# Performance work log

Measured on AMD Instinct MI355X. Metric: run time of the kernel, lower is better.

Reference implementation:

```python
import jax, jax.numpy as jnp
import numpy as np

B, D, C, P = 1024, 768, 150, 64  # batch, in_feats, num_labels, proj2 dim
POS_M, NEG_M = 0.7, 1.4


def setup_inputs() -> dict:
    key = jax.random.key(0)
    ks = jax.random.split(key, 8)
    return {
        "x": jax.random.normal(ks[0], (B, D), jnp.float32),
        "lb": jax.random.randint(ks[1], (B,), 0, C + 1),
        "mem": jax.random.normal(ks[2], (C, D), jnp.float32),
        "fc_w": jax.random.normal(ks[3], (2 * D, 2 * D), jnp.float32) * 0.02,
        "fc_b": jnp.zeros((2 * D,), jnp.float32),
        "p1_w": jax.random.normal(ks[4], (1, 2 * D), jnp.float32) * 0.02,
        "p1_b": jnp.zeros((1,), jnp.float32),
        "p2_w": jax.random.normal(ks[5], (P, 2 * D), jnp.float32) * 0.02,
        "p2_b": jnp.zeros((P,), jnp.float32),
    }


def reference(x, lb, mem, fc_w, fc_b, p1_w, p1_b, p2_w, p2_b):
    d = x.shape[1]
    # cat([a, b], 1) @ fc_w.T == a @ Wx.T + b @ Wm.T  (exact split of the linear)
    Wx, Wm = fc_w[:, :d], fc_w[:, d:]
    xh = x @ Wx.T + fc_b                                # [B, 2D]

    # --- get_logit ---
    seen_h = jax.nn.relu(xh[:, None, :] + mem @ Wm.T)   # [B, C, 2D]
    seen = jnp.einsum('bce,e->bc', seen_h, p1_w[0]) + p1_b[0]   # [B, C]
    uh = jax.nn.relu(xh)                                # cat([x, zeros]) path
    unseen = uh @ p1_w.T + p1_b                         # [B, 1]
    logits = jnp.concatenate([seen, unseen], axis=1)    # [B, C+1]

    # --- masked log-softmax losses (pos_adapte) ---
    labels = jax.nn.one_hot(lb, C + 1, dtype=jnp.float32)
    th = jnp.zeros_like(labels).at[:, -1].set(1.0)
    labels = labels.at[:, -1].set(0.0)
    p_mask = labels + th
    n_mask = 1.0 - labels
    BIG = 1e30
    loss1 = -(jax.nn.log_softmax(logits - (1.0 - p_mask) * BIG, -1) * labels).sum(1)
    loss2 = -(jax.nn.log_softmax(logits - (1.0 - n_mask) * BIG, -1) * th).sum(1)
    loss_cls = (loss1 + loss2).mean()

    # --- metric loss on unseen embedding ---
    u = uh @ p2_w.T + p2_b                              # [B, 64]
    u = u / jnp.maximum(jnp.linalg.norm(u, axis=1, keepdims=True), 1e-12)
    sq_n = (u * u).sum(1)
    sq = sq_n[:, None] + sq_n[None, :] - 2.0 * (u @ u.T)
    err = sq <= 0.0
    dist = jnp.sqrt(jnp.clip(sq, 1e-16, None)) * (~err).astype(u.dtype)
    same = lb[:, None] == lb[None, :]
    eye = jnp.eye(dist.shape[0], dtype=bool)
    pos = (same & ~eye).astype(dist.dtype)
    neg = (~same).astype(dist.dtype)
    pos_l = (jax.nn.relu(dist - POS_M) * pos).sum() / jnp.maximum(pos.sum(), 1.0)
    neg_l = (jax.nn.relu(NEG_M - dist) * neg).sum() / jnp.maximum(neg.sum(), 1.0)

    return loss_cls + pos_l + neg_l
```

## Files before the change

### kernel.cpp

```cpp
#include <hip/hip_runtime.h>
#include <math.h>

#define B_    1024
#define D_    768
#define C_    150
#define P_    64
#define TWOD  1536
#define NCLS  151
#define CPAD  256

#define ECHUNKS 16
#define ECHUNK  96

#define ASTR  40
#define USTRU 120
#define USTR  72

#define OFF_MH      0
#define OFF_XH      (OFF_MH + (C_ * TWOD) / 2)
#define OFF_PARTIAL (OFF_XH + (B_ * TWOD) / 2)
#define OFF_UHF     (OFF_PARTIAL + ECHUNKS * B_ * CPAD)
#define OFF_SQN     (OFF_UHF + (B_ * P_) / 2)
#define OFF_CLS     (OFF_SQN + B_)
#define OFF_PAIR    (OFF_CLS + B_)
#define OFF_XBF     (OFF_PAIR + 1024)
#define OFF_MEMBF   (OFF_XBF + (B_ * D_) / 2)
#define OFF_WBF     (OFF_MEMBF + (C_ * D_) / 2)
#define OFF_P2H     (OFF_WBF + (TWOD * TWOD) / 2)
#define OFF_P1H     (OFF_P2H + (P_ * TWOD) / 2)

typedef __bf16    bfx8   __attribute__((ext_vector_type(8)));
typedef _Float16  fp16x8 __attribute__((ext_vector_type(8)));
typedef _Float16  h2v    __attribute__((ext_vector_type(2)));
typedef float     f32x4  __attribute__((ext_vector_type(4)));

__device__ inline ushort f2bf(float f) {
    union { float f; unsigned u; } c; c.f = f;
    unsigned r = c.u + 0x7fffu + ((c.u >> 16) & 1u);
    return (ushort)(r >> 16);
}
__device__ inline ushort f2h(float f) {
    _Float16 h = (_Float16)f;
    return __builtin_bit_cast(ushort, h);
}
__device__ inline unsigned addrelu2(unsigned a, unsigned m) {
    h2v s = __builtin_bit_cast(h2v, a) + __builtin_bit_cast(h2v, m);
    h2v z = {(_Float16)0.f, (_Float16)0.f};
    s = __builtin_elementwise_max(s, z);
    return __builtin_bit_cast(unsigned, s);
}
__device__ inline unsigned relu2(unsigned a) {
    h2v s = __builtin_bit_cast(h2v, a);
    h2v z = {(_Float16)0.f, (_Float16)0.f};
    s = __builtin_elementwise_max(s, z);
    return __builtin_bit_cast(unsigned, s);
}
__device__ inline float dot2acc(unsigned a, unsigned b, float c) {
    return __builtin_amdgcn_fdot2(__builtin_bit_cast(h2v, a),
                                  __builtin_bit_cast(h2v, b), c, false);
}

#define X4   (B_ * D_ / 4)
#define MEM4 (C_ * D_ / 4)
#define W4   (TWOD * TWOD / 4)
#define P24  (P_ * TWOD / 4)
#define P14  (TWOD / 4)
#define TOT4 (X4 + MEM4 + W4 + P24 + P14)

__global__ __launch_bounds__(256) void prep_cvt(
    const float* __restrict__ x, const float* __restrict__ mem,
    const float* __restrict__ w, const float* __restrict__ p2w,
    const float* __restrict__ p1w,
    ushort* __restrict__ xb, ushort* __restrict__ memb,
    ushort* __restrict__ wb, ushort* __restrict__ p2h,
    ushort* __restrict__ p1h)
{
    int i = blockIdx.x * 256 + threadIdx.x;
    if (i >= TOT4) return;
    const float* src; ushort* dst; int off; bool bf;
    if (i < X4)                        { src = x;   dst = xb;   off = i; bf = true; }
    else if (i < X4 + MEM4)            { src = mem; dst = memb; off = i - X4; bf = true; }
    else if (i < X4 + MEM4 + W4)       { src = w;   dst = wb;   off = i - X4 - MEM4; bf = true; }
    else if (i < X4 + MEM4 + W4 + P24) { src = p2w; dst = p2h;  off = i - X4 - MEM4 - W4; bf = false; }
    else                               { src = p1w; dst = p1h;  off = i - X4 - MEM4 - W4 - P24; bf = false; }
    float4 v = ((const float4*)src)[off];
    ushort4 o;
    if (bf) { o.x = f2bf(v.x); o.y = f2bf(v.y); o.z = f2bf(v.z); o.w = f2bf(v.w); }
    else    { o.x = f2h(v.x);  o.y = f2h(v.y);  o.z = f2h(v.z);  o.w = f2h(v.w); }
    ((ushort4*)dst)[off] = o;
}

__global__ __launch_bounds__(256) void gemm_all(
    const ushort* __restrict__ xbf, const ushort* __restrict__ membf,
    const ushort* __restrict__ wbf, const float* __restrict__ fc_b,
    ushort* __restrict__ xh, ushort* __restrict__ mh)
{
    __shared__ ushort As[64 * ASTR];
    __shared__ ushort Bs[128 * ASTR];
    const int id = blockIdx.x;
    const int t  = threadIdx.x;

    const ushort* A; ushort* Out; int M, m0, n0, koff; bool xblk;
    if (id < 192) {
        xblk = true;  A = xbf;  Out = xh; M = B_;
        m0 = (id & 15) * 64; n0 = (id >> 4) * 128; koff = 0;
    } else {
        int q = id - 192;
        xblk = false; A = membf; Out = mh; M = C_;
        m0 = (q % 3) * 64; n0 = (q / 3) * 128; koff = D_;
    }

    const int wave = t >> 6, lane = t & 63;
    const int wm = (wave & 1) * 32, wn = (wave >> 1) * 64;
    const int fm = lane & 15, quad = lane >> 4;

    const int row_a = t >> 2, qa = (t & 3) * 8;
    const int ar = min(m0 + row_a, M - 1);
    const ushort* Arow = A + (size_t)ar * D_ + qa;
    const ushort* Brow = wbf + (size_t)(n0 + row_a) * TWOD + koff + qa;

    f32x4 acc[2][4];
#pragma unroll
    for (int j = 0; j < 4; ++j) {
        float bv = xblk ? fc_b[n0 + wn + j * 16 + fm] : 0.f;
#pragma unroll
        for (int i = 0; i < 2; ++i)
            acc[i][j] = (f32x4){bv, bv, bv, bv};
    }

    uint4 pa  = *(const uint4*)(Arow);
    uint4 pb0 = *(const uint4*)(Brow);
    uint4 pb1 = *(const uint4*)(Brow + 64 * TWOD);

    for (int k0 = 0; k0 < D_; k0 += 32) {
        __syncthreads();
        *(uint4*)&As[row_a * ASTR + qa] = pa;
        *(uint4*)&Bs[row_a * ASTR + qa] = pb0;
        *(uint4*)&Bs[(64 + row_a) * ASTR + qa] = pb1;
        __syncthreads();
        if (k0 + 32 < D_) {
            pa  = *(const uint4*)(Arow + k0 + 32);
            pb0 = *(const uint4*)(Brow + k0 + 32);
            pb1 = *(const uint4*)(Brow + 64 * TWOD + k0 + 32);
        }
        bfx8 af[2], bf[4];
#pragma unroll
        for (int i = 0; i < 2; ++i)
            af[i] = *(const bfx8*)&As[(wm + i * 16 + fm) * ASTR + quad * 8];
#pragma unroll
        for (int j = 0; j < 4; ++j)
            bf[j] = *(const bfx8*)&Bs[(wn + j * 16 + fm) * ASTR + quad * 8];
#pragma unroll
        for (int i = 0; i < 2; ++i)
#pragma unroll
            for (int j = 0; j < 4; ++j)
                acc[i][j] = __builtin_amdgcn_mfma_f32_16x16x32_bf16(
                    af[i], bf[j], acc[i][j], 0, 0, 0);
    }

#pragma unroll
    for (int i = 0; i < 2; ++i)
#pragma unroll
        for (int j = 0; j < 4; ++j)
#pragma unroll
            for (int r = 0; r < 4; ++r) {
                int row = m0 + wm + i * 16 + quad * 4 + r;
                int col = n0 + wn + j * 16 + fm;
                if (row < M) Out[(size_t)row * TWOD + col] = f2h(acc[i][j][r]);
            }
}

__global__ __launch_bounds__(256) void fused_tile(
    const ushort* __restrict__ xh, const ushort* __restrict__ mh,
    const ushort* __restrict__ p1h, const ushort* __restrict__ p2h,
    float* __restrict__ partial)
{
    __shared__ __align__(16) char smem[46080];
    const int t  = threadIdx.x;
    const int b0 = blockIdx.x * 128;
    const int z  = blockIdx.z;
    const int e0 = z * ECHUNK;

    if (blockIdx.y == 3) {
        ushort* Au = (ushort*)smem;
        ushort* Wu = (ushort*)(smem + 30720);
        const int wave = t >> 6, lane = t & 63;
        const int fm = lane & 15, quad = lane >> 4;

        {
            const int row = t >> 1, kh = (t & 1) * 48;
            const ushort* src = xh + (size_t)(b0 + row) * TWOD + e0 + kh;
            uint4 v[6];
#pragma unroll
            for (int i = 0; i < 6; ++i) v[i] = *(const uint4*)&src[i * 8];
#pragma unroll
            for (int i = 0; i < 6; ++i) {
                v[i].x = relu2(v[i].x); v[i].y = relu2(v[i].y);
                v[i].z = relu2(v[i].z); v[i].w = relu2(v[i].w);
                *(uint4*)&Au[row * USTRU + kh + i * 8] = v[i];
            }
        }
        {
            const int row = t >> 2, ks = (t & 3) * 24;
            const ushort* pw = p2h + (size_t)row * TWOD + e0 + ks;
#pragma unroll
            for (int i = 0; i < 3; ++i)
                *(uint4*)&Wu[row * USTRU + ks + i * 8] = *(const uint4*)&pw[i * 8];
        }
        __syncthreads();

        f32x4 uacc[2][4];
#pragma unroll
        for (int i = 0; i < 2; ++i)
#pragma unroll
            for (int j = 0; j < 4; ++j) uacc[i][j] = (f32x4){0.f, 0.f, 0.f, 0.f};
#pragma unroll
        for (int k0 = 0; k0 < ECHUNK; k0 += 32) {
            fp16x8 af[2], bf[4];
#pragma unroll
            for (int i = 0; i < 2; ++i)
                af[i] = *(const fp16x8*)&Au[(wave * 32 + i * 16 + fm) * USTRU + k0 + quad * 8];
#pragma unroll
            for (int j = 0; j < 4; ++j)
                bf[j] = *(const fp16x8*)&Wu[(j * 16 + fm) * USTRU + k0 + quad * 8];
#pragma unroll
            for (int i = 0; i < 2; ++i)
#pragma unroll
                for (int j = 0; j < 4; ++j)
                    uacc[i][j] = __builtin_amdgcn_mfma_f32_16x16x32_f16(
                        af[i], bf[j], uacc[i][j], 0, 0, 0);
        }
#pragma unroll
        for (int i = 0; i < 2; ++i)
#pragma unroll
            for (int j = 0; j < 4; ++j)
#pragma unroll
                for (int r = 0; r < 4; ++r) {
                    int row = b0 + wave * 32 + i * 16 + quad * 4 + r;
                    partial[((size_t)z * B_ + row) * CPAD + 192 + j * 16 + fm] =
                        uacc[i][j][r];
                }
        return;
    }

    unsigned* xT = (unsigned*)smem;
    unsigned* mT = (unsigned*)(smem + 24576);
    unsigned* wT = (unsigned*)(smem + 36864);
    const int c0 = blockIdx.y * 64;
    const int tm = t & 15, tn = t >> 4;

    {
        const int row = t >> 1, ph = (t & 1) * 48;
        const ushort* src = xh + (size_t)(b0 + row) * TWOD + e0 + ph;
        uint4 v[6];
#pragma unroll
        for (int i = 0; i < 6; ++i) v[i] = *(const uint4*)&src[i * 8];
#pragma unroll
        for (int i = 0; i < 6; ++i) {
            const int ep = (t & 1) * 24 + i * 4;
            xT[(ep + 0) * 128 + row] = v[i].x;
            xT[(ep + 1) * 128 + row] = v[i].y;
            xT[(ep + 2) * 128 + row] = v[i].z;
            xT[(ep + 3) * 128 + row] = v[i].w;
        }
    }
    {
        const int col = t & 63, seg = t >> 6;
        const int gc  = c0 + col;
        uint4 v[3];
        if (gc < C_) {
            const ushort* src = mh + (size_t)gc * TWOD + e0 + seg * 24;
#pragma unroll
            for (int i = 0; i < 3; ++i) v[i] = *(const uint4*)&src[i * 8];
        } else {
#pragma unroll
            for (int i = 0; i < 3; ++i) v[i] = make_uint4(0, 0, 0, 0);
        }
#pragma unroll
        for (int i = 0; i < 3; ++i) {
            const int ep = seg * 12 + i * 4;
            mT[(ep + 0) * 64 + col] = v[i].x;
            mT[(ep + 1) * 64 + col] = v[i].y;
            mT[(ep + 2) * 64 + col] = v[i].z;
            mT[(ep + 3) * 64 + col] = v[i].w;
        }
    }
    if (t < 12) {
        uint4 v = *(const uint4*)&p1h[e0 + t * 8];
        wT[t * 4 + 0] = v.x; wT[t * 4 + 1] = v.y;
        wT[t * 4 + 2] = v.z; wT[t * 4 + 3] = v.w;
    }
    __syncthreads();

    float acc[8][4] = {};
#pragma unroll 4
    for (int ep = 0; ep < 48; ++ep) {
        uint4 a0 = *(const uint4*)&xT[ep * 128 + tm * 8];
        uint4 a1 = *(const uint4*)&xT[ep * 128 + tm * 8 + 4];
        uint4 mj = *(const uint4*)&mT[ep * 64 + tn * 4];
        const unsigned wv = wT[ep];
        const unsigned aa[8] = {a0.x, a0.y, a0.z, a0.w, a1.x, a1.y, a1.z, a1.w};
        const unsigned mm[4] = {mj.x, mj.y, mj.z, mj.w};
#pragma unroll
        for (int i = 0; i < 8; ++i)
#pragma unroll
            for (int j = 0; j < 4; ++j)
                acc[i][j] = dot2acc(addrelu2(aa[i], mm[j]), wv, acc[i][j]);
    }

#pragma unroll
    for (int i = 0; i < 8; ++i) {
        const int gb = b0 + tm * 8 + i;
        float4 v = make_float4(acc[i][0], acc[i][1], acc[i][2], acc[i][3]);
        *(float4*)&partial[((size_t)z * B_ + gb) * CPAD + c0 + tn * 4] = v;
    }
}

__global__ __launch_bounds__(256) void reduce_row(
    const float* __restrict__ partial,
    const float* __restrict__ p1b, const float* __restrict__ p2b,
    const int* __restrict__ lb,
    ushort* __restrict__ uhf, float* __restrict__ sqn,
    float* __restrict__ clsbuf)
{
    const int b = blockIdx.x, t = threadIdx.x;
    float v = 0.f;
#pragma unroll
    for (int z = 0; z < ECHUNKS; ++z)
        v += partial[((size_t)z * B_ + b) * CPAD + t];
    if (t < NCLS)       v += p1b[0];
    else if (t >= 192)  v += p2b[t - 192];

    __shared__ float sval[256];
    sval[t] = v;
    __syncthreads();

    if (t < 64) {
        float uv = sval[192 + t];
        float s = uv * uv;
#pragma unroll
        for (int off = 32; off; off >>= 1) s += __shfl_xor(s, off);
        float inv = 1.f / fmaxf(sqrtf(s), 1e-12f);
        uhf[(size_t)b * P_ + t] = f2h(uv * inv);
        if (t == 0) sqn[b] = s * inv * inv;

        const int l = lb[b];
        float mx = -1e30f;
        for (int j = t; j < NCLS; j += 64)
            if (!(j == l && l < C_)) mx = fmaxf(mx, sval[j]);
#pragma unroll
        for (int off = 32; off; off >>= 1) mx = fmaxf(mx, __shfl_xor(mx, off));
        float se = 0.f;
        for (int j = t; j < NCLS; j += 64)
            if (!(j == l && l < C_)) se += expf(sval[j] - mx);
#pragma unroll
        for (int off = 32; off; off >>= 1) se += __shfl_xor(se, off);

        if (t == 0) {
            float l150  = sval[C_];
            float loss2 = mx + logf(se) - l150;
            float loss1 = 0.f;
            if (l < C_) {
                float a  = sval[l];
                float m2 = fmaxf(a, l150);
                loss1 = m2 - a + logf(expf(a - m2) + expf(l150 - m2));
            }
            clsbuf[b] = loss1 + loss2;
        }
    }
}

__global__ __launch_bounds__(256) void pair_loss(
    const ushort* __restrict__ uhf, const float* __restrict__ sqn,
    const int* __restrict__ lb, float* __restrict__ pairpart)
{
    __shared__ ushort ui_s[64 * USTR];
    __shared__ ushort uj_s[64 * USTR];
    __shared__ float sni[64], snj[64];
    __shared__ int   li[64],  lj[64];
    __shared__ float red[4][4];

    const int t  = threadIdx.x;
    const int i0 = blockIdx.x * 64, j0 = blockIdx.y * 64;

    for (int idx = t; idx < 512; idx += 256) {
        int row = idx >> 3, ch = (idx & 7) * 8;
        *(uint4*)&ui_s[row * USTR + ch] =
            *(const uint4*)&uhf[(size_t)(i0 + row) * P_ + ch];
        *(uint4*)&uj_s[row * USTR + ch] =
            *(const uint4*)&uhf[(size_t)(j0 + row) * P_ + ch];
    }
    if (t < 64)       { sni[t] = sqn[i0 + t]; li[t] = lb[i0 + t]; }
    else if (t < 128) { int q = t - 64; snj[q] = sqn[j0 + q]; lj[q] = lb[j0 + q]; }
    __syncthreads();

    const int wave = t >> 6, lane = t & 63;
    const int n = lane & 15, quad = lane >> 4;
    const int iw = wave * 16;

    const fp16x8 af0 = *(const fp16x8*)&ui_s[(iw + n) * USTR + quad * 8];
    const fp16x8 af1 = *(const fp16x8*)&ui_s[(iw + n) * USTR + quad * 8 + 32];

    f32x4 acc[4];
#pragma unroll
    for (int jt = 0; jt < 4; ++jt) {
        const fp16x8 bf0 = *(const fp16x8*)&uj_s[(jt * 16 + n) * USTR + quad * 8];
        const fp16x8 bf1 = *(const fp16x8*)&uj_s[(jt * 16 + n) * USTR + quad * 8 + 32];
        acc[jt] = __builtin_amdgcn_mfma_f32_16x16x32_f16(
            af0, bf0, (f32x4){0.f, 0.f, 0.f, 0.f}, 0, 0, 0);
        acc[jt] = __builtin_amdgcn_mfma_f32_16x16x32_f16(
            af1, bf1, acc[jt], 0, 0, 0);
    }

    float ps = 0.f, pc = 0.f, ns = 0.f, nc = 0.f;
#pragma unroll
    for (int jt = 0; jt < 4; ++jt)
#pragma unroll
        for (int r = 0; r < 4; ++r) {
            const int il = iw + quad * 4 + r;
            const int jl = jt * 16 + n;
            float sq = sni[il] + snj[jl] - 2.f * acc[jt][r];
            float dist = sq > 0.f ? sqrtf(fmaxf(sq, 1e-16f)) : 0.f;
            bool same = (li[il] == lj[jl]);
            if (same) {
                if (i0 + il != j0 + jl) { ps += fmaxf(dist - 0.7f, 0.f); pc += 1.f; }
            } else {
                ns += fmaxf(1.4f - dist, 0.f); nc += 1.f;
            }
        }

#pragma unroll
    for (int off = 32; off; off >>= 1) {
        ps += __shfl_xor(ps, off); pc += __shfl_xor(pc, off);
        ns += __shfl_xor(ns, off); nc += __shfl_xor(nc, off);
    }
    if (lane == 0) { red[0][wave] = ps; red[1][wave] = pc;
                     red[2][wave] = ns; red[3][wave] = nc; }
    __syncthreads();
    if (t == 0) {
        float4 v;
        v.x = red[0][0] + red[0][1] + red[0][2] + red[0][3];
        v.y = red[1][0] + red[1][1] + red[1][2] + red[1][3];
        v.z = red[2][0] + red[2][1] + red[2][2] + red[2][3];
        v.w = red[3][0] + red[3][1] + red[3][2] + red[3][3];
        *(float4*)&pairpart[(size_t)(blockIdx.y * 16 + blockIdx.x) * 4] = v;
    }
}

__global__ __launch_bounds__(256) void finalize(
    const float* __restrict__ clsbuf, const float* __restrict__ pairpart,
    float* __restrict__ out)
{
    __shared__ float red[5][4];
    const int t = threadIdx.x;
    float c = clsbuf[t] + clsbuf[t + 256] + clsbuf[t + 512] + clsbuf[t + 768];
    float4 pp = *(const float4*)&pairpart[(size_t)t * 4];
    float ps = pp.x, pc = pp.y, ns = pp.z, nc = pp.w;
#pragma unroll
    for (int off = 32; off; off >>= 1) {
        c  += __shfl_xor(c, off);
        ps += __shfl_xor(ps, off); pc += __shfl_xor(pc, off);
        ns += __shfl_xor(ns, off); nc += __shfl_xor(nc, off);
    }
    const int wave = t >> 6, lane = t & 63;
    if (lane == 0) { red[0][wave] = c; red[1][wave] = ps; red[2][wave] = pc;
                     red[3][wave] = ns; red[4][wave] = nc; }
    __syncthreads();
    if (t == 0) {
        float C = 0.f, PS = 0.f, PC = 0.f, NS = 0.f, NC = 0.f;
#pragma unroll
        for (int w = 0; w < 4; ++w) {
            C += red[0][w]; PS += red[1][w]; PC += red[2][w];
            NS += red[3][w]; NC += red[4][w];
        }
        out[0] = C / (float)B_ + PS / fmaxf(PC, 1.f) + NS / fmaxf(NC, 1.f);
    }
}

extern "C" void kernel_launch(void* const* d_in, const int* in_sizes, int n_in,
                              void* d_out, int out_size, void* d_ws, size_t ws_size,
                              hipStream_t stream)
{
    const float* x    = (const float*)d_in[0];
    const int*   lb   = (const int*)d_in[1];
    const float* mem  = (const float*)d_in[2];
    const float* fc_w = (const float*)d_in[3];
    const float* fc_b = (const float*)d_in[4];
    const float* p1w  = (const float*)d_in[5];
    const float* p1b  = (const float*)d_in[6];
    const float* p2w  = (const float*)d_in[7];
    const float* p2b  = (const float*)d_in[8];

    float* ws       = (float*)d_ws;
    ushort* mh      = (ushort*)(ws + OFF_MH);
    ushort* xh      = (ushort*)(ws + OFF_XH);
    float* partials = ws + OFF_PARTIAL;
    ushort* uhf     = (ushort*)(ws + OFF_UHF);
    float* sqn      = ws + OFF_SQN;
    float* clsbuf   = ws + OFF_CLS;
    float* pairpart = ws + OFF_PAIR;
    ushort* xbf     = (ushort*)(ws + OFF_XBF);
    ushort* membf   = (ushort*)(ws + OFF_MEMBF);
    ushort* wbf     = (ushort*)(ws + OFF_WBF);
    ushort* p2h     = (ushort*)(ws + OFF_P2H);
    ushort* p1h     = (ushort*)(ws + OFF_P1H);

    prep_cvt<<<(TOT4 + 255) / 256, 256, 0, stream>>>(x, mem, fc_w, p2w, p1w,
                                                     xbf, membf, wbf, p2h, p1h);
    gemm_all<<<228, 256, 0, stream>>>(xbf, membf, wbf, fc_b, xh, mh);
    fused_tile<<<dim3(8, 4, ECHUNKS), 256, 0, stream>>>(xh, mh, p1h, p2h,
                                                        partials);
    reduce_row<<<B_, 256, 0, stream>>>(partials, p1b, p2b, lb, uhf, sqn, clsbuf);
    pair_loss<<<dim3(16, 16), 256, 0, stream>>>(uhf, sqn, lb, pairpart);
    finalize<<<1, 256, 0, stream>>>(clsbuf, pairpart, (float*)d_out);
}
```

Measured before the change: 129.8 us.

## Fuse all six kernels into one persistent kernel with grid barriers

```diff
diff --git a/kernel.cpp b/kernel.cpp
--- a/kernel.cpp
+++ b/kernel.cpp
@@ -15,6 +15,8 @@
 #define ASTR  40
 #define USTRU 120
 #define USTR  72
+
+#define NBLK  512
 
 #define OFF_MH      0
 #define OFF_XH      (OFF_MH + (C_ * TWOD) / 2)
@@ -28,6 +30,7 @@
 #define OFF_WBF     (OFF_MEMBF + (C_ * D_) / 2)
 #define OFF_P2H     (OFF_WBF + (TWOD * TWOD) / 2)
 #define OFF_P1H     (OFF_P2H + (P_ * TWOD) / 2)
+#define OFF_BAR     (OFF_P1H + TWOD / 2)
 
 typedef __bf16    bfx8   __attribute__((ext_vector_type(8)));
 typedef _Float16  fp16x8 __attribute__((ext_vector_type(8)));
@@ -58,6 +61,35 @@
 __device__ inline float dot2acc(unsigned a, unsigned b, float c) {
     return __builtin_amdgcn_fdot2(__builtin_bit_cast(h2v, a),
                                   __builtin_bit_cast(h2v, b), c, false);
+}
+
+__device__ __forceinline__ void grid_barrier(int* bar)
+{
+    __syncthreads();
+    if (threadIdx.x == 0) {
+        int* gen = bar + 1;
+        const int g = __hip_atomic_load(gen, __ATOMIC_RELAXED,
+                                        __HIP_MEMORY_SCOPE_AGENT);
+        int* gcnt = bar + 16 + (blockIdx.x >> 4) * 16;
+        int gv = __hip_atomic_fetch_add(gcnt, 1, __ATOMIC_ACQ_REL,
+                                        __HIP_MEMORY_SCOPE_AGENT);
+        if (gv == 15) {
+            __hip_atomic_store(gcnt, 0, __ATOMIC_RELAXED,
+                               __HIP_MEMORY_SCOPE_AGENT);
+            int rv = __hip_atomic_fetch_add(bar, 1, __ATOMIC_ACQ_REL,
+                                            __HIP_MEMORY_SCOPE_AGENT);
+            if (rv == 31) {
+                __hip_atomic_store(bar, 0, __ATOMIC_RELAXED,
+                                   __HIP_MEMORY_SCOPE_AGENT);
+                __hip_atomic_fetch_add(gen, 1, __ATOMIC_RELEASE,
+                                       __HIP_MEMORY_SCOPE_AGENT);
+            }
+        }
+        while (__hip_atomic_load(gen, __ATOMIC_ACQUIRE,
+                                 __HIP_MEMORY_SCOPE_AGENT) == g)
+            __builtin_amdgcn_s_sleep(1);
+    }
+    __syncthreads();
 }
 
 #define X4   (B_ * D_ / 4)
@@ -67,7 +99,7 @@
 #define P14  (TWOD / 4)
 #define TOT4 (X4 + MEM4 + W4 + P24 + P14)
 
-__global__ __launch_bounds__(256) void prep_cvt(
+__device__ __forceinline__ void phase_cvt(
     const float* __restrict__ x, const float* __restrict__ mem,
     const float* __restrict__ w, const float* __restrict__ p2w,
     const float* __restrict__ p1w,
@@ -75,30 +107,31 @@
     ushort* __restrict__ wb, ushort* __restrict__ p2h,
     ushort* __restrict__ p1h)
 {
-    int i = blockIdx.x * 256 + threadIdx.x;
-    if (i >= TOT4) return;
-    const float* src; ushort* dst; int off; bool bf;
-    if (i < X4)                        { src = x;   dst = xb;   off = i; bf = true; }
-    else if (i < X4 + MEM4)            { src = mem; dst = memb; off = i - X4; bf = true; }
-    else if (i < X4 + MEM4 + W4)       { src = w;   dst = wb;   off = i - X4 - MEM4; bf = true; }
-    else if (i < X4 + MEM4 + W4 + P24) { src = p2w; dst = p2h;  off = i - X4 - MEM4 - W4; bf = false; }
-    else                               { src = p1w; dst = p1h;  off = i - X4 - MEM4 - W4 - P24; bf = false; }
-    float4 v = ((const float4*)src)[off];
-    ushort4 o;
-    if (bf) { o.x = f2bf(v.x); o.y = f2bf(v.y); o.z = f2bf(v.z); o.w = f2bf(v.w); }
-    else    { o.x = f2h(v.x);  o.y = f2h(v.y);  o.z = f2h(v.z);  o.w = f2h(v.w); }
-    ((ushort4*)dst)[off] = o;
-}
-
-__global__ __launch_bounds__(256) void gemm_all(
+    for (int i = blockIdx.x * 256 + threadIdx.x; i < TOT4; i += NBLK * 256) {
+        const float* src; ushort* dst; int off; bool bf;
+        if (i < X4)                        { src = x;   dst = xb;   off = i; bf = true; }
+        else if (i < X4 + MEM4)            { src = mem; dst = memb; off = i - X4; bf = true; }
+        else if (i < X4 + MEM4 + W4)       { src = w;   dst = wb;   off = i - X4 - MEM4; bf = true; }
+        else if (i < X4 + MEM4 + W4 + P24) { src = p2w; dst = p2h;  off = i - X4 - MEM4 - W4; bf = false; }
+        else                               { src = p1w; dst = p1h;  off = i - X4 - MEM4 - W4 - P24; bf = false; }
+        float4 v = ((const float4*)src)[off];
+        ushort4 o;
+        if (bf) { o.x = f2bf(v.x); o.y = f2bf(v.y); o.z = f2bf(v.z); o.w = f2bf(v.w); }
+        else    { o.x = f2h(v.x);  o.y = f2h(v.y);  o.z = f2h(v.z);  o.w = f2h(v.w); }
+        ((ushort4*)dst)[off] = o;
+    }
+}
+
+__device__ __forceinline__ void phase_gemm(
+    int id, char* smemc,
     const ushort* __restrict__ xbf, const ushort* __restrict__ membf,
     const ushort* __restrict__ wbf, const float* __restrict__ fc_b,
     ushort* __restrict__ xh, ushort* __restrict__ mh)
 {
-    __shared__ ushort As[64 * ASTR];
-    __shared__ ushort Bs[128 * ASTR];
-    const int id = blockIdx.x;
-    const int t  = threadIdx.x;
+    if (id >= 228) return;
+    ushort* As = (ushort*)smemc;
+    ushort* Bs = (ushort*)(smemc + 64 * ASTR * 2);
+    const int t = threadIdx.x;
 
     const ushort* A; ushort* Out; int M, m0, n0, koff; bool xblk;
     if (id < 192) {
@@ -143,19 +176,19 @@
             pb0 = *(const uint4*)(Brow + k0 + 32);
             pb1 = *(const uint4*)(Brow + 64 * TWOD + k0 + 32);
         }
-        bfx8 af[2], bf[4];
+        bfx8 af[2], bff[4];
 #pragma unroll
         for (int i = 0; i < 2; ++i)
             af[i] = *(const bfx8*)&As[(wm + i * 16 + fm) * ASTR + quad * 8];
 #pragma unroll
         for (int j = 0; j < 4; ++j)
-            bf[j] = *(const bfx8*)&Bs[(wn + j * 16 + fm) * ASTR + quad * 8];
+            bff[j] = *(const bfx8*)&Bs[(wn + j * 16 + fm) * ASTR + quad * 8];
 #pragma unroll
         for (int i = 0; i < 2; ++i)
 #pragma unroll
             for (int j = 0; j < 4; ++j)
                 acc[i][j] = __builtin_amdgcn_mfma_f32_16x16x32_bf16(
-                    af[i], bf[j], acc[i][j], 0, 0, 0);
+                    af[i], bff[j], acc[i][j], 0, 0, 0);
     }
 
 #pragma unroll
@@ -170,18 +203,19 @@
             }
 }
 
-__global__ __launch_bounds__(256) void fused_tile(
+__device__ __forceinline__ void phase_fused(
+    int id, char* smem,
     const ushort* __restrict__ xh, const ushort* __restrict__ mh,
     const ushort* __restrict__ p1h, const ushort* __restrict__ p2h,
     float* __restrict__ partial)
 {
-    __shared__ __align__(16) char smem[46080];
     const int t  = threadIdx.x;
-    const int b0 = blockIdx.x * 128;
-    const int z  = blockIdx.z;
+    const int b0 = (id & 7) * 128;
+    const int y  = (id >> 3) & 3;
+    const int z  = id >> 5;
     const int e0 = z * ECHUNK;
 
-    if (blockIdx.y == 3) {
+    if (y == 3) {
         ushort* Au = (ushort*)smem;
         ushort* Wu = (ushort*)(smem + 30720);
         const int wave = t >> 6, lane = t & 63;
@@ -216,19 +250,19 @@
             for (int j = 0; j < 4; ++j) uacc[i][j] = (f32x4){0.f, 0.f, 0.f, 0.f};
 #pragma unroll
         for (int k0 = 0; k0 < ECHUNK; k0 += 32) {
-            fp16x8 af[2], bf[4];
+            fp16x8 af[2], bff[4];
 #pragma unroll
             for (int i = 0; i < 2; ++i)
                 af[i] = *(const fp16x8*)&Au[(wave * 32 + i * 16 + fm) * USTRU + k0 + quad * 8];
 #pragma unroll
             for (int j = 0; j < 4; ++j)
-                bf[j] = *(const fp16x8*)&Wu[(j * 16 + fm) * USTRU + k0 + quad * 8];
+                bff[j] = *(const fp16x8*)&Wu[(j * 16 + fm) * USTRU + k0 + quad * 8];
 #pragma unroll
             for (int i = 0; i < 2; ++i)
 #pragma unroll
                 for (int j = 0; j < 4; ++j)
                     uacc[i][j] = __builtin_amdgcn_mfma_f32_16x16x32_f16(
-                        af[i], bf[j], uacc[i][j], 0, 0, 0);
+                        af[i], bff[j], uacc[i][j], 0, 0, 0);
         }
 #pragma unroll
         for (int i = 0; i < 2; ++i)
@@ -246,7 +280,7 @@
     unsigned* xT = (unsigned*)smem;
     unsigned* mT = (unsigned*)(smem + 24576);
     unsigned* wT = (unsigned*)(smem + 36864);
-    const int c0 = blockIdx.y * 64;
+    const int c0 = y * 64;
     const int tm = t & 15, tn = t >> 4;
 
     {
@@ -316,72 +350,80 @@
     }
 }
 
-__global__ __launch_bounds__(256) void reduce_row(
+__device__ __forceinline__ void phase_reduce(
+    char* smemc,
     const float* __restrict__ partial,
     const float* __restrict__ p1b, const float* __restrict__ p2b,
     const int* __restrict__ lb,
     ushort* __restrict__ uhf, float* __restrict__ sqn,
     float* __restrict__ clsbuf)
 {
-    const int b = blockIdx.x, t = threadIdx.x;
-    float v = 0.f;
-#pragma unroll
-    for (int z = 0; z < ECHUNKS; ++z)
-        v += partial[((size_t)z * B_ + b) * CPAD + t];
-    if (t < NCLS)       v += p1b[0];
-    else if (t >= 192)  v += p2b[t - 192];
-
-    __shared__ float sval[256];
-    sval[t] = v;
-    __syncthreads();
-
-    if (t < 64) {
-        float uv = sval[192 + t];
-        float s = uv * uv;
-#pragma unroll
-        for (int off = 32; off; off >>= 1) s += __shfl_xor(s, off);
-        float inv = 1.f / fmaxf(sqrtf(s), 1e-12f);
-        uhf[(size_t)b * P_ + t] = f2h(uv * inv);
-        if (t == 0) sqn[b] = s * inv * inv;
-
-        const int l = lb[b];
-        float mx = -1e30f;
-        for (int j = t; j < NCLS; j += 64)
-            if (!(j == l && l < C_)) mx = fmaxf(mx, sval[j]);
-#pragma unroll
-        for (int off = 32; off; off >>= 1) mx = fmaxf(mx, __shfl_xor(mx, off));
-        float se = 0.f;
-        for (int j = t; j < NCLS; j += 64)
-            if (!(j == l && l < C_)) se += expf(sval[j] - mx);
-#pragma unroll
-        for (int off = 32; off; off >>= 1) se += __shfl_xor(se, off);
-
-        if (t == 0) {
-            float l150  = sval[C_];
-            float loss2 = mx + logf(se) - l150;
-            float loss1 = 0.f;
-            if (l < C_) {
-                float a  = sval[l];
-                float m2 = fmaxf(a, l150);
-                loss1 = m2 - a + logf(expf(a - m2) + expf(l150 - m2));
+    float* sval = (float*)smemc;
+    const int t = threadIdx.x;
+    for (int b = blockIdx.x; b < B_; b += NBLK) {
+        float v = 0.f;
+#pragma unroll
+        for (int z = 0; z < ECHUNKS; ++z)
+            v += partial[((size_t)z * B_ + b) * CPAD + t];
+        if (t < NCLS)       v += p1b[0];
+        else if (t >= 192)  v += p2b[t - 192];
+
+        sval[t] = v;
+        __syncthreads();
+
+        if (t < 64) {
+            float uv = sval[192 + t];
+            float s = uv * uv;
+#pragma unroll
+            for (int off = 32; off; off >>= 1) s += __shfl_xor(s, off);
+            float inv = 1.f / fmaxf(sqrtf(s), 1e-12f);
+            uhf[(size_t)b * P_ + t] = f2h(uv * inv);
+            if (t == 0) sqn[b] = s * inv * inv;
+
+            const int l = lb[b];
+            float mx = -1e30f;
+            for (int j = t; j < NCLS; j += 64)
+                if (!(j == l && l < C_)) mx = fmaxf(mx, sval[j]);
+#pragma unroll
+            for (int off = 32; off; off >>= 1) mx = fmaxf(mx, __shfl_xor(mx, off));
+            float se = 0.f;
+            for (int j = t; j < NCLS; j += 64)
+                if (!(j == l && l < C_)) se += expf(sval[j] - mx);
+#pragma unroll
+            for (int off = 32; off; off >>= 1) se += __shfl_xor(se, off);
+
+            if (t == 0) {
+                float l150  = sval[C_];
+                float loss2 = mx + logf(se) - l150;
+                float loss1 = 0.f;
+                if (l < C_) {
+                    float a  = sval[l];
+                    float m2 = fmaxf(a, l150);
+                    loss1 = m2 - a + logf(expf(a - m2) + expf(l150 - m2));
+                }
+                clsbuf[b] = loss1 + loss2;
             }
-            clsbuf[b] = loss1 + loss2;
-        }
-    }
-}
-
-__global__ __launch_bounds__(256) void pair_loss(
+        }
+        __syncthreads();
+    }
+}
+
+__device__ __forceinline__ void phase_pair(
+    int id, char* smemc,
     const ushort* __restrict__ uhf, const float* __restrict__ sqn,
     const int* __restrict__ lb, float* __restrict__ pairpart)
 {
-    __shared__ ushort ui_s[64 * USTR];
-    __shared__ ushort uj_s[64 * USTR];
-    __shared__ float sni[64], snj[64];
-    __shared__ int   li[64],  lj[64];
-    __shared__ float red[4][4];
+    if (id >= 256) return;
+    ushort* ui_s = (ushort*)smemc;
+    ushort* uj_s = (ushort*)(smemc + 9216);
+    float*  sni  = (float*)(smemc + 18432);
+    float*  snj  = (float*)(smemc + 18688);
+    int*    li   = (int*)(smemc + 18944);
+    int*    lj   = (int*)(smemc + 19200);
+    float*  red  = (float*)(smemc + 19456);
 
     const int t  = threadIdx.x;
-    const int i0 = blockIdx.x * 64, j0 = blockIdx.y * 64;
+    const int i0 = (id & 15) * 64, j0 = (id >> 4) * 64;
 
     for (int idx = t; idx < 512; idx += 256) {
         int row = idx >> 3, ch = (idx & 7) * 8;
@@ -434,24 +476,26 @@
         ps += __shfl_xor(ps, off); pc += __shfl_xor(pc, off);
         ns += __shfl_xor(ns, off); nc += __shfl_xor(nc, off);
     }
-    if (lane == 0) { red[0][wave] = ps; red[1][wave] = pc;
-                     red[2][wave] = ns; red[3][wave] = nc; }
+    if (lane == 0) { red[0 * 4 + wave] = ps; red[1 * 4 + wave] = pc;
+                     red[2 * 4 + wave] = ns; red[3 * 4 + wave] = nc; }
     __syncthreads();
     if (t == 0) {
         float4 v;
-        v.x = red[0][0] + red[0][1] + red[0][2] + red[0][3];
-        v.y = red[1][0] + red[1][1] + red[1][2] + red[1][3];
-        v.z = red[2][0] + red[2][1] + red[2][2] + red[2][3];
-        v.w = red[3][0] + red[3][1] + red[3][2] + red[3][3];
-        *(float4*)&pairpart[(size_t)(blockIdx.y * 16 + blockIdx.x) * 4] = v;
-    }
-}
-
-__global__ __launch_bounds__(256) void finalize(
+        v.x = red[0] + red[1] + red[2] + red[3];
+        v.y = red[4] + red[5] + red[6] + red[7];
+        v.z = red[8] + red[9] + red[10] + red[11];
+        v.w = red[12] + red[13] + red[14] + red[15];
+        *(float4*)&pairpart[(size_t)id * 4] = v;
+    }
+}
+
+__device__ __forceinline__ void phase_final(
+    char* smemc,
     const float* __restrict__ clsbuf, const float* __restrict__ pairpart,
     float* __restrict__ out)
 {
-    __shared__ float red[5][4];
+    if (blockIdx.x != 0) return;
+    float* red = (float*)smemc;
     const int t = threadIdx.x;
     float c = clsbuf[t] + clsbuf[t + 256] + clsbuf[t + 512] + clsbuf[t + 768];
     float4 pp = *(const float4*)&pairpart[(size_t)t * 4];
@@ -463,18 +507,58 @@
         ns += __shfl_xor(ns, off); nc += __shfl_xor(nc, off);
     }
     const int wave = t >> 6, lane = t & 63;
-    if (lane == 0) { red[0][wave] = c; red[1][wave] = ps; red[2][wave] = pc;
-                     red[3][wave] = ns; red[4][wave] = nc; }
+    if (lane == 0) { red[0 * 4 + wave] = c; red[1 * 4 + wave] = ps;
+                     red[2 * 4 + wave] = pc; red[3 * 4 + wave] = ns;
+                     red[4 * 4 + wave] = nc; }
     __syncthreads();
     if (t == 0) {
         float C = 0.f, PS = 0.f, PC = 0.f, NS = 0.f, NC = 0.f;
 #pragma unroll
         for (int w = 0; w < 4; ++w) {
-            C += red[0][w]; PS += red[1][w]; PC += red[2][w];
-            NS += red[3][w]; NC += red[4][w];
+            C += red[0 * 4 + w]; PS += red[1 * 4 + w]; PC += red[2 * 4 + w];
+            NS += red[3 * 4 + w]; NC += red[4 * 4 + w];
         }
         out[0] = C / (float)B_ + PS / fmaxf(PC, 1.f) + NS / fmaxf(NC, 1.f);
     }
+}
+
+__global__ __launch_bounds__(256, 2) void mega(
+    const float* __restrict__ x, const int* __restrict__ lb,
+    const float* __restrict__ mem, const float* __restrict__ fc_w,
+    const float* __restrict__ fc_b, const float* __restrict__ p1w,
+    const float* __restrict__ p1b, const float* __restrict__ p2w,
+    const float* __restrict__ p2b,
+    float* ws, float* out)
+{
+    __shared__ __align__(16) char smem[46080];
+
+    ushort* mh       = (ushort*)(ws + OFF_MH);
+    ushort* xh       = (ushort*)(ws + OFF_XH);
+    float*  partial  = ws + OFF_PARTIAL;
+    ushort* uhf      = (ushort*)(ws + OFF_UHF);
+    float*  sqn      = ws + OFF_SQN;
+    float*  clsbuf   = ws + OFF_CLS;
+    float*  pairpart = ws + OFF_PAIR;
+    ushort* xbf      = (ushort*)(ws + OFF_XBF);
+    ushort* membf    = (ushort*)(ws + OFF_MEMBF);
+    ushort* wbf      = (ushort*)(ws + OFF_WBF);
+    ushort* p2h      = (ushort*)(ws + OFF_P2H);
+    ushort* p1h      = (ushort*)(ws + OFF_P1H);
+    int*    bar      = (int*)(ws + OFF_BAR);
+
+    const int id = blockIdx.x;
+
+    phase_cvt(x, mem, fc_w, p2w, p1w, xbf, membf, wbf, p2h, p1h);
+    grid_barrier(bar);
+    phase_gemm(id, smem, xbf, membf, wbf, fc_b, xh, mh);
+    grid_barrier(bar);
+    phase_fused(id, smem, xh, mh, p1h, p2h, partial);
+    grid_barrier(bar);
+    phase_reduce(smem, partial, p1b, p2b, lb, uhf, sqn, clsbuf);
+    grid_barrier(bar);
+    phase_pair(id, smem, uhf, sqn, lb, pairpart);
+    grid_barrier(bar);
+    phase_final(smem, clsbuf, pairpart, out);
 }
 
 extern "C" void kernel_launch(void* const* d_in, const int* in_sizes, int n_in,
@@ -491,26 +575,11 @@
     const float* p2w  = (const float*)d_in[7];
     const float* p2b  = (const float*)d_in[8];
 
-    float* ws       = (float*)d_ws;
-    ushort* mh      = (ushort*)(ws + OFF_MH);
-    ushort* xh      = (ushort*)(ws + OFF_XH);
-    float* partials = ws + OFF_PARTIAL;
-    ushort* uhf     = (ushort*)(ws + OFF_UHF);
-    float* sqn      = ws + OFF_SQN;
-    float* clsbuf   = ws + OFF_CLS;
-    float* pairpart = ws + OFF_PAIR;
-    ushort* xbf     = (ushort*)(ws + OFF_XBF);
-    ushort* membf   = (ushort*)(ws + OFF_MEMBF);
-    ushort* wbf     = (ushort*)(ws + OFF_WBF);
-    ushort* p2h     = (ushort*)(ws + OFF_P2H);
-    ushort* p1h     = (ushort*)(ws + OFF_P1H);
-
-    prep_cvt<<<(TOT4 + 255) / 256, 256, 0, stream>>>(x, mem, fc_w, p2w, p1w,
-                                                     xbf, membf, wbf, p2h, p1h);
-    gemm_all<<<228, 256, 0, stream>>>(xbf, membf, wbf, fc_b, xh, mh);
-    fused_tile<<<dim3(8, 4, ECHUNKS), 256, 0, stream>>>(xh, mh, p1h, p2h,
-                                                        partials);
-    reduce_row<<<B_, 256, 0, stream>>>(partials, p1b, p2b, lb, uhf, sqn, clsbuf);
-    pair_loss<<<dim3(16, 16), 256, 0, stream>>>(uhf, sqn, lb, pairpart);
-    finalize<<<1, 256, 0, stream>>>(clsbuf, pairpart, (float*)d_out);
-}
+    float* ws  = (float*)d_ws;
+    int*   bar = (int*)(ws + OFF_BAR);
+
+    hipMemsetAsync(bar, 0, 4096, stream);
+
+    mega<<<NBLK, 256, 0, stream>>>(x, lb, mem, fc_w, fc_b,
+                                   p1w, p1b, p2w, p2b, ws, (float*)d_out);
+}
```

Result: slower. 400.9 us (+208.8%).
